# Kernel tuning notes

Measured on AMD Instinct MI355X. Metric: run time of the kernel, lower is better.

Reference implementation:

```python
import jax, jax.numpy as jnp
import numpy as np

N_NODES = 100000
N_EDGES = 1600000
D_IN = 64
D_OUT = 64


def _sage_conv(x, Wl, b, Wr, src, dst, inv_deg):
    # mean-aggregate neighbor features: gather x[src], scatter-sum into dst, divide by degree
    agg = jax.ops.segment_sum(x[src], dst, num_segments=N_NODES)  # [N, d]
    agg = agg * inv_deg                                            # mean with deg clamped >= 1
    # PyG SAGEConv: lin_l(agg) (with bias) + lin_r(x) (no bias)
    return agg @ Wl.T + b + x @ Wr.T


def setup_inputs() -> dict:
    key = jax.random.key(0)
    ks = jax.random.split(key, 8)
    x = jax.random.normal(ks[0], (N_NODES, D_IN), dtype=jnp.float32)
    edge_index = jax.random.randint(ks[1], (2, N_EDGES), 0, N_NODES, dtype=jnp.int64)
    s1 = 1.0 / np.sqrt(D_IN)
    s2 = 1.0 / np.sqrt(D_OUT)
    Wl1 = jax.random.uniform(ks[2], (D_OUT, D_IN), jnp.float32, -s1, s1)
    b1 = jnp.zeros((D_OUT,), jnp.float32)
    Wr1 = jax.random.uniform(ks[3], (D_OUT, D_IN), jnp.float32, -s1, s1)
    Wl2 = jax.random.uniform(ks[4], (D_OUT, D_OUT), jnp.float32, -s2, s2)
    b2 = jnp.zeros((D_OUT,), jnp.float32)
    Wr2 = jax.random.uniform(ks[5], (D_OUT, D_OUT), jnp.float32, -s2, s2)
    return {"x": x, "edge_index": edge_index, "Wl1": Wl1, "b1": b1, "Wr1": Wr1,
            "Wl2": Wl2, "b2": b2, "Wr2": Wr2}


def reference(x, edge_index, Wl1, b1, Wr1, Wl2, b2, Wr2):
    src, dst = edge_index[0], edge_index[1]
    deg = jax.ops.segment_sum(jnp.ones((N_EDGES,), jnp.float32), dst, num_segments=N_NODES)
    inv_deg = (1.0 / jnp.maximum(deg, 1.0))[:, None]  # [N, 1]
    h = _sage_conv(x, Wl1, b1, Wr1, src, dst, inv_deg)
    h = _sage_conv(h, Wl2, b2, Wr2, src, dst, inv_deg)
    return h
```

## Files before the change

kernel.cpp:

```cpp
#include <hip/hip_runtime.h>
#include <hip/hip_bf16.h>

#define NN 100000
#define NE 1600000
#define NB 196
#define BCAP 9216
#define BIN_CHUNK 4096
#define BIN_BLKS ((NE + BIN_CHUNK - 1) / BIN_CHUNK)

typedef __attribute__((ext_vector_type(8))) short bf16x8;
typedef __attribute__((ext_vector_type(4))) float f32x4;

__device__ inline unsigned short f2bf(float f) {
    union { __hip_bfloat16 h; unsigned short u; } c;
    c.h = __float2bfloat16(f);
    return c.u;
}

__device__ inline unsigned f2e4m3(float f) {
    unsigned u = __float_as_uint(f);
    unsigned s = (u >> 24) & 0x80u;
    unsigned b = u & 0x7FFFFFFFu;
    float af = __uint_as_float(b);
    if (af >= 464.f) return s | 0x7Eu;
    if (af < 0.015625f) {
        unsigned m = (unsigned)__float2int_rn(af * 512.f);
        return s | m;
    }
    unsigned r = b + 0x7FFFFu + ((b >> 20) & 1u);
    int e = (int)(r >> 23) - 127;
    if (e > 8) return s | 0x7Eu;
    return s | ((unsigned)(e + 7) << 3) | ((r >> 20) & 7u);
}

#if __has_builtin(__builtin_amdgcn_cvt_f32_fp8)
#define FP8CVT(w, k) __builtin_amdgcn_cvt_f32_fp8((int)(w), (k))
#else
__device__ inline float fp8_manual(unsigned b) {
    unsigned v = ((b & 0x80u) << 24) | ((b & 0x7Fu) << 20);
    return __uint_as_float(v) * 0x1p120f;
}
#define FP8CVT(w, k) fp8_manual(((w) >> ((k) * 8)) & 0xFFu)
#endif

__global__ __launch_bounds__(256) void k_prep(const float* __restrict__ x,
                                              unsigned short* __restrict__ xb,
                                              unsigned char* __restrict__ x8,
                                              const float* __restrict__ Wl1,
                                              const float* __restrict__ Wr1,
                                              const float* __restrict__ Wl2,
                                              const float* __restrict__ Wr2,
                                              unsigned short* __restrict__ Wc1,
                                              unsigned short* __restrict__ Wc2,
                                              int* __restrict__ gcur) {
    int i = blockIdx.x * 256 + threadIdx.x;
    if (i < NB) gcur[i] = i * BCAP;
    if (i < 4096) {
        int fo = i >> 6, k = i & 63;
        Wc1[fo * 128 + k]      = f2bf(Wl1[i]);
        Wc1[fo * 128 + 64 + k] = f2bf(Wr1[i]);
        Wc2[fo * 128 + k]      = f2bf(Wl2[i]);
        Wc2[fo * 128 + 64 + k] = f2bf(Wr2[i]);
    }
    if (i < NN * 64 / 8) {
        const float4* p = (const float4*)(x + (size_t)i * 8);
        float4 v0 = p[0], v1 = p[1];
        union { bf16x8 v; unsigned short u[8]; } c;
        c.u[0] = f2bf(v0.x); c.u[1] = f2bf(v0.y); c.u[2] = f2bf(v0.z); c.u[3] = f2bf(v0.w);
        c.u[4] = f2bf(v1.x); c.u[5] = f2bf(v1.y); c.u[6] = f2bf(v1.z); c.u[7] = f2bf(v1.w);
        *(bf16x8*)(xb + (size_t)i * 8) = c.v;
        unsigned lo = f2e4m3(v0.x) | (f2e4m3(v0.y) << 8) |
                      (f2e4m3(v0.z) << 16) | (f2e4m3(v0.w) << 24);
        unsigned hi = f2e4m3(v1.x) | (f2e4m3(v1.y) << 8) |
                      (f2e4m3(v1.z) << 16) | (f2e4m3(v1.w) << 24);
        *(uint2*)(x8 + (size_t)i * 8) = make_uint2(lo, hi);
    }
}

__global__ __launch_bounds__(256) void k_bin(const int* __restrict__ src,
                                             const int* __restrict__ dst,
                                             int* __restrict__ gcur,
                                             unsigned* __restrict__ binned) {
    __shared__ int hist[NB];
    __shared__ int base[NB];
    __shared__ int lcur[NB];
    const int t = threadIdx.x;
    const int e0 = blockIdx.x * BIN_CHUNK;
    const int n4 = min(BIN_CHUNK, NE - e0) >> 2;
    for (int i = t; i < NB; i += 256) { hist[i] = 0; lcur[i] = 0; }
    __syncthreads();
    const int4* d4p = (const int4*)(dst + e0);
    const int4* s4p = (const int4*)(src + e0);
    for (int i = t; i < n4; i += 256) {
        int4 d = d4p[i];
        atomicAdd(&hist[d.x >> 9], 1);
        atomicAdd(&hist[d.y >> 9], 1);
        atomicAdd(&hist[d.z >> 9], 1);
        atomicAdd(&hist[d.w >> 9], 1);
    }
    __syncthreads();
    for (int i = t; i < NB; i += 256) {
        int h = hist[i];
        base[i] = h ? atomicAdd(&gcur[i], h) : 0;
    }
    __syncthreads();
    for (int i = t; i < n4; i += 256) {
        int4 d = d4p[i];
        int4 s = s4p[i];
        #define PLACE(dd, ss) {                                         \
            int b = (dd) >> 9;                                          \
            int p = base[b] + atomicAdd(&lcur[b], 1);                   \
            binned[p] = ((unsigned)((dd) & 511) << 17) | (unsigned)(ss);}
        PLACE(d.x, s.x) PLACE(d.y, s.y) PLACE(d.z, s.z) PLACE(d.w, s.w)
        #undef PLACE
    }
}

__global__ __launch_bounds__(256) void k_csr(const int* __restrict__ gcur,
                                             unsigned* __restrict__ binned,
                                             int2* __restrict__ noff,
                                             float* __restrict__ inv) {
    __shared__ unsigned buf[BCAP];
    __shared__ int h[512];
    __shared__ int off[512];
    __shared__ int lcur[512];
    __shared__ int s[256];
    const int b = blockIdx.x;
    const int t = threadIdx.x;
    const int base = b * BCAP;
    const int cnt = min(gcur[b] - base, BCAP);
    for (int i = t; i < 512; i += 256) h[i] = 0;
    __syncthreads();
    for (int i = t; i < cnt; i += 256) {
        unsigned v = binned[base + i];
        buf[i] = v;
        atomicAdd(&h[v >> 17], 1);
    }
    __syncthreads();
    int a0 = h[2 * t], a1 = h[2 * t + 1];
    s[t] = a0 + a1;
    __syncthreads();
    #pragma unroll
    for (int o = 1; o < 256; o <<= 1) {
        int u = (t >= o) ? s[t - o] : 0;
        __syncthreads();
        s[t] += u;
        __syncthreads();
    }
    int ex = s[t] - (a0 + a1);
    off[2 * t] = ex;          lcur[2 * t] = ex;
    off[2 * t + 1] = ex + a0; lcur[2 * t + 1] = ex + a0;
    __syncthreads();
    for (int i = t; i < cnt; i += 256) {
        unsigned v = buf[i];
        int dl = v >> 17;
        int p = atomicAdd(&lcur[dl], 1);
        binned[base + p] = v & 0x1FFFFu;
    }
    #pragma unroll
    for (int q = 0; q < 2; ++q) {
        int l = 2 * t + q;
        int node = b * 512 + l;
        if (node < NN) {
            int st = base + off[l];
            noff[node] = make_int2(st, st + h[l]);
            inv[node] = 1.0f / fmaxf((float)h[l], 1.0f);
        }
    }
}

__global__ __launch_bounds__(512) void k_fused(const unsigned short* __restrict__ feat,
                                               const unsigned char* __restrict__ f8,
                                               const int2* __restrict__ noff,
                                               const unsigned* __restrict__ csr,
                                               const float* __restrict__ inv,
                                               const unsigned short* __restrict__ Wc,
                                               const float* __restrict__ bias,
                                               float* __restrict__ Cf,
                                               unsigned short* __restrict__ Cb,
                                               unsigned char* __restrict__ C8) {
    __shared__ unsigned short sA[64 * 72];
    const int t = threadIdx.x;
    const int n0 = blockIdx.x * 64;

    {
        const int g = t >> 3;
        const int p = t & 7;
        const int node = n0 + g;
        float a[8] = {0.f, 0.f, 0.f, 0.f, 0.f, 0.f, 0.f, 0.f};
        float iv = 0.f;
        if (node < NN) {
            int2 oe = noff[node];
            int beg = oe.x, end = oe.y;
            iv = inv[node];

            #define UNPK8(u)                                           \
                a[0] += FP8CVT((u).x, 0); a[1] += FP8CVT((u).x, 1);    \
                a[2] += FP8CVT((u).x, 2); a[3] += FP8CVT((u).x, 3);    \
                a[4] += FP8CVT((u).y, 0); a[5] += FP8CVT((u).y, 1);    \
                a[6] += FP8CVT((u).y, 2); a[7] += FP8CVT((u).y, 3);
            #define GATHER(s) (*(const uint2*)(f8 + (size_t)(s) * 64 + p * 8))

            int j = beg;
            uint2 u0, u1, u2, u3;
            bool pending = false;
            if (j + 4 <= end) {
                u0 = GATHER(csr[j]);     u1 = GATHER(csr[j + 1]);
                u2 = GATHER(csr[j + 2]); u3 = GATHER(csr[j + 3]);
                j += 4;
                pending = true;
            }
            for (; j + 4 <= end; j += 4) {
                uint2 v0 = GATHER(csr[j]);     uint2 v1 = GATHER(csr[j + 1]);
                uint2 v2 = GATHER(csr[j + 2]); uint2 v3 = GATHER(csr[j + 3]);
                UNPK8(u0) UNPK8(u1) UNPK8(u2) UNPK8(u3)
                u0 = v0; u1 = v1; u2 = v2; u3 = v3;
            }
            if (pending) { UNPK8(u0) UNPK8(u1) UNPK8(u2) UNPK8(u3) }
            for (; j < end; ++j) {
                uint2 w0 = GATHER(csr[j]);
                UNPK8(w0)
            }
            #undef GATHER
            #undef UNPK8
        }
        union { bf16x8 v; unsigned short u[8]; } c;
        #pragma unroll
        for (int e = 0; e < 8; ++e) c.u[e] = f2bf(a[e] * iv);
        *(bf16x8*)(&sA[g * 72 + p * 8]) = c.v;
    }
    __syncthreads();

    const int w = t >> 6;
    const int l = t & 63;
    const int cn = l & 15;
    const int ks = l >> 4;
    const int s = w & 3;
    const int h = w >> 2;
    const int lrow = s * 16 + cn;
    const int arow = n0 + lrow;
    const int aclamp = (arow < NN) ? arow : 0;

    f32x4 acc0 = {0.f, 0.f, 0.f, 0.f};
    f32x4 acc1 = {0.f, 0.f, 0.f, 0.f};

    #pragma unroll
    for (int kb = 0; kb < 4; ++kb) {
        bf16x8 aa;
        if (kb < 2) aa = *(const bf16x8*)(&sA[lrow * 72 + kb * 32 + ks * 8]);
        else        aa = *(const bf16x8*)(feat + (size_t)aclamp * 64 + (kb - 2) * 32 + ks * 8);
        const unsigned short* wb = Wc + cn * 128 + kb * 32 + ks * 8;
        bf16x8 b0 = *(const bf16x8*)(wb + (size_t)(2 * h) * 16 * 128);
        bf16x8 b1 = *(const bf16x8*)(wb + (size_t)(2 * h + 1) * 16 * 128);
        acc0 = __builtin_amdgcn_mfma_f32_16x16x32_bf16(aa, b0, acc0, 0, 0, 0);
        acc1 = __builtin_amdgcn_mfma_f32_16x16x32_bf16(aa, b1, acc1, 0, 0, 0);
    }

    #pragma unroll
    for (int fb = 0; fb < 2; ++fb) {
        f32x4 av = fb ? acc1 : acc0;
        int f = 2 * h + fb;
        float bv = bias[f * 16 + cn];
        #pragma unroll
        for (int r = 0; r < 4; ++r) {
            int node = n0 + s * 16 + ks * 4 + r;
            if (node < NN) {
                float val = av[r] + bv;
                if (Cb) {
                    Cb[(size_t)node * 64 + f * 16 + cn] = f2bf(val);
                    C8[(size_t)node * 64 + f * 16 + cn] = (unsigned char)f2e4m3(val);
                } else {
                    Cf[(size_t)node * 64 + f * 16 + cn] = val;
                }
            }
        }
    }
}


extern "C" void kernel_launch(void* const* d_in, const int* in_sizes, int n_in,
                              void* d_out, int out_size, void* d_ws, size_t ws_size,
                              hipStream_t stream) {
    const float* x   = (const float*)d_in[0];
    const int*   ei  = (const int*)d_in[1];
    const int*   src = ei;
    const int*   dst = ei + NE;
    const float* Wl1 = (const float*)d_in[2];
    const float* b1  = (const float*)d_in[3];
    const float* Wr1 = (const float*)d_in[4];
    const float* Wl2 = (const float*)d_in[5];
    const float* b2  = (const float*)d_in[6];
    const float* Wr2 = (const float*)d_in[7];
    float* out = (float*)d_out;

    char* ws = (char*)d_ws;
    size_t off = 0;
    auto alloc = [&](size_t bytes) {
        void* p = ws + off;
        off = (off + bytes + 255) & ~(size_t)255;
        return p;
    };
    unsigned short* xb     = (unsigned short*)alloc(2 * (size_t)NN * 64);
    unsigned short* h1b    = (unsigned short*)alloc(2 * (size_t)NN * 64);
    unsigned char*  x8     = (unsigned char*)alloc((size_t)NN * 64);
    unsigned char*  h18    = (unsigned char*)alloc((size_t)NN * 64);
    unsigned*       binned = (unsigned*)alloc(sizeof(unsigned) * NB * BCAP);
    int2*           noff   = (int2*)alloc(sizeof(int2) * NN);
    float*          inv    = (float*)alloc(sizeof(float) * NN);
    int*            gcur   = (int*)alloc(sizeof(int) * NB);
    unsigned short* Wc1    = (unsigned short*)alloc(2 * 64 * 128);
    unsigned short* Wc2    = (unsigned short*)alloc(2 * 64 * 128);

    k_prep<<<(NN * 64 / 8 + 255) / 256, 256, 0, stream>>>(x, xb, x8, Wl1, Wr1, Wl2, Wr2,
                                                          Wc1, Wc2, gcur);
    k_bin <<<BIN_BLKS, 256, 0, stream>>>(src, dst, gcur, binned);
    k_csr <<<NB, 256, 0, stream>>>(gcur, binned, noff, inv);

    k_fused<<<(NN + 63) / 64, 512, 0, stream>>>(xb, x8, noff, binned, inv, Wc1, b1,
                                                (float*)nullptr, h1b, h18);
    k_fused<<<(NN + 63) / 64, 512, 0, stream>>>(h1b, h18, noff, binned, inv, Wc2, b2,
                                                out, (unsigned short*)nullptr,
                                                (unsigned char*)nullptr);
}
```

Measured before the change: 141.1 us.

## Balance edge gather across threads with merge-path split and LDS atomic accumulation

Result: slower. 220.8 us (+56.5%).

```diff
diff --git a/kernel.cpp b/kernel.cpp
--- a/kernel.cpp
+++ b/kernel.cpp
@@ -124,7 +124,7 @@
     __shared__ int h[512];
     __shared__ int off[512];
     __shared__ int lcur[512];
-    __shared__ int s[256];
+    __shared__ int sc[256];
     const int b = blockIdx.x;
     const int t = threadIdx.x;
     const int base = b * BCAP;
@@ -138,16 +138,16 @@
     }
     __syncthreads();
     int a0 = h[2 * t], a1 = h[2 * t + 1];
-    s[t] = a0 + a1;
+    sc[t] = a0 + a1;
     __syncthreads();
     #pragma unroll
     for (int o = 1; o < 256; o <<= 1) {
-        int u = (t >= o) ? s[t - o] : 0;
+        int u = (t >= o) ? sc[t - o] : 0;
         __syncthreads();
-        s[t] += u;
+        sc[t] += u;
         __syncthreads();
     }
-    int ex = s[t] - (a0 + a1);
+    int ex = sc[t] - (a0 + a1);
     off[2 * t] = ex;          lcur[2 * t] = ex;
     off[2 * t + 1] = ex + a0; lcur[2 * t + 1] = ex + a0;
     __syncthreads();
@@ -179,55 +179,88 @@
                                                float* __restrict__ Cf,
                                                unsigned short* __restrict__ Cb,
                                                unsigned char* __restrict__ C8) {
+    __shared__ float accF[64 * 68];
+    __shared__ int sEnds[64];
     __shared__ unsigned short sA[64 * 72];
     const int t = threadIdx.x;
     const int n0 = blockIdx.x * 64;
+    const int valid = min(64, NN - n0);
+
+    if (t < 64) {
+        int i = (t < valid) ? t : (valid - 1);
+        sEnds[t] = noff[n0 + i].y;
+    }
+    for (int i = t; i < 64 * 68; i += 512) accF[i] = 0.f;
+    __syncthreads();
+
+    const int estart = noff[n0].x;
+    const int eend = sEnds[63];
+    const int E = eend - estart;
 
     {
         const int g = t >> 3;
         const int p = t & 7;
-        const int node = n0 + g;
-        float a[8] = {0.f, 0.f, 0.f, 0.f, 0.f, 0.f, 0.f, 0.f};
-        float iv = 0.f;
-        if (node < NN) {
-            int2 oe = noff[node];
-            int beg = oe.x, end = oe.y;
-            iv = inv[node];
-
-            #define UNPK8(u)                                           \
+        const int cpg = (E + 63) >> 6;
+        int gbeg = estart + g * cpg;
+        int gend = min(gbeg + cpg, eend);
+        if (gbeg < gend) {
+            int lo = 0, hi = 63;
+            while (lo < hi) {
+                int mid = (lo + hi) >> 1;
+                if (gbeg < sEnds[mid]) hi = mid; else lo = mid + 1;
+            }
+            int cur = lo;
+            int curEnd = sEnds[cur];
+            float a[8] = {0.f, 0.f, 0.f, 0.f, 0.f, 0.f, 0.f, 0.f};
+
+            #define FLUSH() {                                          \
+                float* rp = accF + cur * 68 + p * 8;                   \
+                atomicAdd(rp + 0, a[0]); atomicAdd(rp + 1, a[1]);      \
+                atomicAdd(rp + 2, a[2]); atomicAdd(rp + 3, a[3]);      \
+                atomicAdd(rp + 4, a[4]); atomicAdd(rp + 5, a[5]);      \
+                atomicAdd(rp + 6, a[6]); atomicAdd(rp + 7, a[7]);      \
+                a[0]=0.f;a[1]=0.f;a[2]=0.f;a[3]=0.f;                   \
+                a[4]=0.f;a[5]=0.f;a[6]=0.f;a[7]=0.f; }
+            #define PROC(jj, u) {                                      \
+                while ((jj) >= curEnd) {                               \
+                    FLUSH();                                           \
+                    ++cur;                                             \
+                    curEnd = sEnds[cur < 64 ? cur : 63];               \
+                }                                                      \
                 a[0] += FP8CVT((u).x, 0); a[1] += FP8CVT((u).x, 1);    \
                 a[2] += FP8CVT((u).x, 2); a[3] += FP8CVT((u).x, 3);    \
                 a[4] += FP8CVT((u).y, 0); a[5] += FP8CVT((u).y, 1);    \
-                a[6] += FP8CVT((u).y, 2); a[7] += FP8CVT((u).y, 3);
+                a[6] += FP8CVT((u).y, 2); a[7] += FP8CVT((u).y, 3); }
             #define GATHER(s) (*(const uint2*)(f8 + (size_t)(s) * 64 + p * 8))
 
-            int j = beg;
-            uint2 u0, u1, u2, u3;
-            bool pending = false;
-            if (j + 4 <= end) {
-                u0 = GATHER(csr[j]);     u1 = GATHER(csr[j + 1]);
-                u2 = GATHER(csr[j + 2]); u3 = GATHER(csr[j + 3]);
-                j += 4;
-                pending = true;
+            int j = gbeg;
+            for (; j + 4 <= gend; j += 4) {
+                uint2 q0 = GATHER(csr[j]);     uint2 q1 = GATHER(csr[j + 1]);
+                uint2 q2 = GATHER(csr[j + 2]); uint2 q3 = GATHER(csr[j + 3]);
+                PROC(j, q0) PROC(j + 1, q1) PROC(j + 2, q2) PROC(j + 3, q3)
             }
-            for (; j + 4 <= end; j += 4) {
-                uint2 v0 = GATHER(csr[j]);     uint2 v1 = GATHER(csr[j + 1]);
-                uint2 v2 = GATHER(csr[j + 2]); uint2 v3 = GATHER(csr[j + 3]);
-                UNPK8(u0) UNPK8(u1) UNPK8(u2) UNPK8(u3)
-                u0 = v0; u1 = v1; u2 = v2; u3 = v3;
+            for (; j < gend; ++j) {
+                uint2 q = GATHER(csr[j]);
+                PROC(j, q)
             }
-            if (pending) { UNPK8(u0) UNPK8(u1) UNPK8(u2) UNPK8(u3) }
-            for (; j < end; ++j) {
-                uint2 w0 = GATHER(csr[j]);
-                UNPK8(w0)
-            }
+            FLUSH();
             #undef GATHER
-            #undef UNPK8
+            #undef PROC
+            #undef FLUSH
         }
+    }
+    __syncthreads();
+
+    {
+        const int n = t >> 3;
+        const int p = t & 7;
+        const int node = n0 + n;
+        float iv = (node < NN) ? inv[node] : 0.f;
+        const float* rp = accF + n * 68 + p * 8;
         union { bf16x8 v; unsigned short u[8]; } c;
         #pragma unroll
-        for (int e = 0; e < 8; ++e) c.u[e] = f2bf(a[e] * iv);
-        *(bf16x8*)(&sA[g * 72 + p * 8]) = c.v;
+        for (int e = 0; e < 8; ++e) c.u[e] = f2bf(rp[e] * iv);
+        *(bf16x8*)(&sA[n * 72 + p * 8]) = c.v;
     }
     __syncthreads();
 
```
